# Performance work log

Measured on AMD Instinct MI355X. Metric: run time of the kernel, lower is better.

## Reference

```python
import jax, jax.numpy as jnp
import numpy as np

DIM, N_HEADS, N_KV_HEADS = 2048, 32, 8
HEAD_DIM = DIM // N_HEADS            # 64
KV_REPEAT = N_HEADS // N_KV_HEADS    # 4
ROPE_THETA = 10000.0


def _rope(x, start_pos):
    # x: [B, T, Hx, hd]  (rotate-half / GPT-NeoX style RoPE)
    B, T, Hx, hd = x.shape
    half = hd // 2
    inv_freq = 1.0 / (ROPE_THETA ** (jnp.arange(half, dtype=jnp.float32) / half))
    pos = (start_pos + jnp.arange(T)).astype(jnp.float32)
    ang = pos[:, None] * inv_freq[None, :]            # [T, half]
    cos = jnp.cos(ang)[None, :, None, :]              # [1, T, 1, half]
    sin = jnp.sin(ang)[None, :, None, :]
    x1, x2 = x[..., :half], x[..., half:]
    return jnp.concatenate([x1 * cos - x2 * sin, x1 * sin + x2 * cos], axis=-1).astype(x.dtype)


def setup_inputs() -> dict:
    key = jax.random.key(0)
    ks = jax.random.split(key, 5)
    B, T = 2, 2048
    s = 1.0 / np.sqrt(DIM)
    return {
        "x": jax.random.normal(ks[0], (B, T, DIM), dtype=jnp.float32),
        "Wq": jax.random.normal(ks[1], (DIM, N_HEADS * HEAD_DIM), dtype=jnp.float32) * s,
        "Wk": jax.random.normal(ks[2], (DIM, N_KV_HEADS * HEAD_DIM), dtype=jnp.float32) * s,
        "Wv": jax.random.normal(ks[3], (DIM, N_KV_HEADS * HEAD_DIM), dtype=jnp.float32) * s,
        "Wo": jax.random.normal(ks[4], (DIM, DIM), dtype=jnp.float32) * s,
        "start_pos": 0,
    }


def reference(x, Wq, Wk, Wv, Wo, start_pos):
    B, T, _ = x.shape
    G, R, hd = N_KV_HEADS, KV_REPEAT, HEAD_DIM
    # projections -> [B, T, H, hd]
    Q = (x @ Wq).reshape(B, T, N_HEADS, hd)
    K = (x @ Wk).reshape(B, T, G, hd)
    V = (x @ Wv).reshape(B, T, G, hd)
    Q = _rope(Q, start_pos)
    K = _rope(K, start_pos)
    # GQA: group query heads as (G kv-groups, R repeats) matching repeat_interleave order
    Qg = Q.reshape(B, T, G, R, hd)
    scale = 1.0 / jnp.sqrt(jnp.asarray(hd, dtype=Q.dtype))
    scores = jnp.einsum('bqgrd,bkgd->bgrqk', Qg, K) * scale   # [B,G,R,T,T]
    # causal mask (is_causal=True since T > 1)
    causal = jnp.tril(jnp.ones((T, T), dtype=bool))
    scores = jnp.where(causal[None, None, None, :, :], scores, jnp.finfo(scores.dtype).min)
    attn = jax.nn.softmax(scores, axis=-1)
    out = jnp.einsum('bgrqk,bkgd->bqgrd', attn, V).reshape(B, T, DIM)
    y = out @ Wo
    # original also returns (K, V) with heads-first layout [B, G, T, hd]
    return (y, K.transpose(0, 2, 1, 3), V.transpose(0, 2, 1, 3))
```

## Files before the change

### kernel.cpp

```cpp
#include <hip/hip_runtime.h>
#include <hip/hip_bf16.h>
#include <stdint.h>


typedef __attribute__((ext_vector_type(4))) float f32x4;
typedef __attribute__((ext_vector_type(16))) float f32x16;
typedef __attribute__((ext_vector_type(8))) short sfrag;
typedef __attribute__((ext_vector_type(8))) __bf16 bfrag;
typedef __attribute__((ext_vector_type(4))) unsigned int u32x4;
typedef unsigned short u16;

__device__ __forceinline__ f32x4 mfma16(sfrag a, sfrag b, f32x4 c) {
  return __builtin_amdgcn_mfma_f32_16x16x32_bf16(
      __builtin_bit_cast(bfrag, a), __builtin_bit_cast(bfrag, b), c, 0, 0, 0);
}
__device__ __forceinline__ f32x16 mfma32(sfrag a, sfrag b, f32x16 c) {
  return __builtin_amdgcn_mfma_f32_32x32x16_bf16(
      __builtin_bit_cast(bfrag, a), __builtin_bit_cast(bfrag, b), c, 0, 0, 0);
}
__device__ __forceinline__ u16 f2b(float f) {
  return __builtin_bit_cast(u16, (__bf16)f);
}
__device__ __forceinline__ unsigned pack2(float a, float b) {
  return (unsigned)f2b(a) | ((unsigned)f2b(b) << 16);
}
__device__ __forceinline__ void swap32(unsigned& a, unsigned& b) {
  asm("v_permlane32_swap_b32 %0, %1" : "+v"(a), "+v"(b));
}

#define GAS __attribute__((address_space(1)))
#define LAS __attribute__((address_space(3)))
__device__ __forceinline__ void gll16(const void* g, void* l) {
  __builtin_amdgcn_global_load_lds((GAS unsigned int*)g, (LAS unsigned int*)l, 16, 0, 0);
}

__global__ __launch_bounds__(256) void k_convx(const float* __restrict__ X,
                                               u16* __restrict__ Y, int n) {
  int i = (blockIdx.x * 256 + threadIdx.x) * 4;
  if (i >= n) return;
  float4 v = *(const float4*)(X + i);
  *(ushort4*)(Y + i) = make_ushort4(f2b(v.x), f2b(v.y), f2b(v.z), f2b(v.w));
}

__global__ __launch_bounds__(256) void k_csn(const int* __restrict__ sp,
                                             float2* __restrict__ csn) {
  const int i = blockIdx.x * 256 + threadIdx.x;
  const int t = i >> 5, j = i & 31;
  const float freq = powf(10000.0f, -(float)j * (1.0f / 32.0f));
  const float ang = (float)(sp[0] + t) * freq;
  csn[i] = make_float2(cosf(ang), sinf(ang));
}

__global__ __launch_bounds__(256) void k_convT3(const float* __restrict__ Wq,
                                                const float* __restrict__ Wk,
                                                const float* __restrict__ Wv,
                                                u16* __restrict__ Wt) {
  __shared__ float tile[64][65];
  const int n0g = blockIdx.x * 64;
  const float* W; int N, n0;
  if (n0g < 2048)      { W = Wq; N = 2048; n0 = n0g; }
  else if (n0g < 2560) { W = Wk; N = 512;  n0 = n0g - 2048; }
  else                 { W = Wv; N = 512;  n0 = n0g - 2560; }
  const int k0 = blockIdx.y * 64;
  #pragma unroll
  for (int p = 0; p < 16; ++p) {
    int idx = p * 256 + threadIdx.x;
    int kk = idx >> 6, nn = idx & 63;
    tile[kk][nn] = W[(size_t)(k0 + kk) * N + n0 + nn];
  }
  __syncthreads();
  #pragma unroll
  for (int p = 0; p < 16; ++p) {
    int idx = p * 256 + threadIdx.x;
    int nn = idx >> 6, kk = idx & 63;
    Wt[(size_t)(n0g + nn) * 2048 + k0 + kk] = f2b(tile[kk][nn]);
  }
}

__global__ __launch_bounds__(256) void k_convT(const float* __restrict__ W,
                                               u16* __restrict__ Wt, int N) {
  __shared__ float tile[64][65];
  int n0 = blockIdx.x * 64, k0 = blockIdx.y * 64;
  #pragma unroll
  for (int p = 0; p < 16; ++p) {
    int idx = p * 256 + threadIdx.x;
    int kk = idx >> 6, nn = idx & 63;
    tile[kk][nn] = W[(size_t)(k0 + kk) * N + n0 + nn];
  }
  __syncthreads();
  #pragma unroll
  for (int p = 0; p < 16; ++p) {
    int idx = p * 256 + threadIdx.x;
    int nn = idx >> 6, kk = idx & 63;
    Wt[(size_t)(n0 + nn) * 2048 + k0 + kk] = f2b(tile[kk][nn]);
  }
}

template<int MODE>
__global__ __launch_bounds__(256, 3) void k_gemm128(const u16* __restrict__ A,
                                                    const u16* __restrict__ Bt,
                                                    float* __restrict__ C,
                                                    int N, int K, int GY,
                                                    const float2* __restrict__ csn,
                                                    u16* __restrict__ Qb,
                                                    u16* __restrict__ Kb,
                                                    float* __restrict__ Kout,
                                                    float* __restrict__ Vout) {
  __shared__ u16 lds[16384];
  char* const L = (char*)&lds[0];
  const int tid = threadIdx.x;
  const int q8 = gridDim.x >> 3;
  const int id2 = (blockIdx.x & 7) * q8 + (blockIdx.x >> 3);
  const int by = id2 % GY, bx = id2 / GY;
  const int wid = tid >> 6, lane = tid & 63;
  const int wm = wid >> 1, wn = wid & 1;
  const int l16 = lane & 15, l4 = lane >> 4;
  const size_t K2 = (size_t)K * 2;
  const char* Ab = (const char*)(A + (size_t)(by * 128) * K);
  const char* Bb = (const char*)(Bt + (size_t)(bx * 128) * K);
  const int NT = K >> 6;

  auto stage = [&](const char* gb, int reg, int t) {
    #pragma unroll
    for (int ld = 0; ld < 4; ++ld) {
      const int p = ld * 4096 + tid * 16;
      const int r = p >> 7;
      const int cb = (p & 127) ^ ((r & 7) << 4);
      gll16(gb + (size_t)r * K2 + (size_t)t * 128 + cb, L + reg + p);
    }
  };

  const int swz = (l16 & 7) << 4;
  const int c0 = (l4 * 16) ^ swz;
  const int c1 = (64 + l4 * 16) ^ swz;
  const int aOff = (wm * 64 + l16) * 128;
  const int bOff = 16384 + (wn * 64 + l16) * 128;

  f32x4 acc[4][4];
  #pragma unroll
  for (int m = 0; m < 4; ++m)
    #pragma unroll
    for (int n = 0; n < 4; ++n) acc[m][n] = f32x4{0.f, 0.f, 0.f, 0.f};

  for (int t = 0; t < NT; ++t) {
    stage(Ab, 0, t);
    stage(Bb, 16384, t);
    __syncthreads();
    sfrag a0[4], a1[4], b0[4], b1[4];
    #pragma unroll
    for (int m = 0; m < 4; ++m) {
      a0[m] = *(const sfrag*)(L + aOff + m * 2048 + c0);
      a1[m] = *(const sfrag*)(L + aOff + m * 2048 + c1);
    }
    #pragma unroll
    for (int n = 0; n < 4; ++n) {
      b0[n] = *(const sfrag*)(L + bOff + n * 2048 + c0);
      b1[n] = *(const sfrag*)(L + bOff + n * 2048 + c1);
    }
    #pragma unroll
    for (int m = 0; m < 4; ++m)
      #pragma unroll
      for (int n = 0; n < 4; ++n) {
        acc[m][n] = mfma16(a0[m], b0[n], acc[m][n]);
        acc[m][n] = mfma16(a1[m], b1[n], acc[m][n]);
      }
    __syncthreads();
  }

  if constexpr (MODE == 0) {
    float* Cb = C + (size_t)(by * 128 + wm * 64) * N + bx * 128 + wn * 64;
    #pragma unroll
    for (int m = 0; m < 4; ++m)
      #pragma unroll
      for (int n = 0; n < 4; ++n)
        #pragma unroll
        for (int r = 0; r < 4; ++r)
          Cb[(size_t)(m * 16 + l4 * 4 + r) * N + n * 16 + l16] = acc[m][n][r];
  } else {
    const int head = bx * 2 + wn;
    const int row0 = by * 128 + wm * 64;
    if (head < 40) {
      const float QS = 0.125f * 1.44269504f;
      #pragma unroll
      for (int m = 0; m < 4; ++m)
        #pragma unroll
        for (int r = 0; r < 4; ++r) {
          const int tg = row0 + m * 16 + l4 * 4 + r;
          const int b = tg >> 11, t = tg & 2047;
          #pragma unroll
          for (int n = 0; n < 2; ++n) {
            const int j = n * 16 + l16;
            const float2 cz = csn[t * 32 + j];
            const float x1 = acc[m][n][r], x2 = acc[m][n + 2][r];
            const float o1 = x1 * cz.x - x2 * cz.y;
            const float o2 = x1 * cz.y + x2 * cz.x;
            if (head < 32) {
              const size_t o = (((size_t)b * 32 + head) * 2048 + t) * 64 + j;
              Qb[o] = f2b(o1 * QS);
              Qb[o + 32] = f2b(o2 * QS);
            } else {
              const int g = head - 32;
              const size_t o = (((size_t)b * 8 + g) * 2048 + t) * 64 + j;
              Kb[o] = f2b(o1);  Kb[o + 32] = f2b(o2);
              Kout[o] = o1;     Kout[o + 32] = o2;
            }
          }
        }
    } else {
      const int g = head - 40;
      #pragma unroll
      for (int m = 0; m < 4; ++m)
        #pragma unroll
        for (int r = 0; r < 4; ++r) {
          const int tg = row0 + m * 16 + l4 * 4 + r;
          const int b = tg >> 11, t = tg & 2047;
          const size_t o = (((size_t)b * 8 + g) * 2048 + t) * 64;
          #pragma unroll
          for (int n = 0; n < 4; ++n)
            Vout[o + n * 16 + l16] = acc[m][n][r];
        }
    }
  }
}

__global__ __launch_bounds__(256) void k_vtrans(const float* __restrict__ Vout,
                                                u16* __restrict__ Vt) {
  __shared__ float tile[64][65];
  int t0 = blockIdx.x * 64;
  int bg = blockIdx.y;
  const float* src = Vout + (size_t)bg * (2048 * 64);
  #pragma unroll
  for (int p = 0; p < 16; ++p) {
    int idx = p * 256 + threadIdx.x;
    int tt = idx >> 6, d = idx & 63;
    tile[tt][d] = src[(size_t)(t0 + tt) * 64 + d];
  }
  __syncthreads();
  #pragma unroll
  for (int p = 0; p < 16; ++p) {
    int idx = p * 256 + threadIdx.x;
    int d = idx >> 6, tt = idx & 63;
    Vt[((size_t)bg * 64 + d) * 2048 + t0 + tt] = f2b(tile[tt][d]);
  }
}

__device__ __forceinline__ void pv4(const float* p, sfrag v0a, sfrag v0b,
                                    sfrag v1a, sfrag v1b,
                                    f32x16& O0, f32x16& O1, float& l) {
  unsigned w[8];
  #pragma unroll
  for (int j = 0; j < 8; ++j) w[j] = pack2(p[2 * j], p[2 * j + 1]);
  swap32(w[0], w[2]);
  swap32(w[1], w[3]);
  swap32(w[4], w[6]);
  swap32(w[5], w[7]);
  const sfrag pf0 = __builtin_bit_cast(sfrag, u32x4{w[0], w[1], w[2], w[3]});
  const sfrag pf1 = __builtin_bit_cast(sfrag, u32x4{w[4], w[5], w[6], w[7]});
  O0 = mfma32(v0a, pf0, O0);
  O0 = mfma32(v0b, pf1, O0);
  O1 = mfma32(v1a, pf0, O1);
  O1 = mfma32(v1b, pf1, O1);
  float s[8];
  #pragma unroll
  for (int j = 0; j < 8; ++j) s[j] = p[j] + p[j + 8];
  #pragma unroll
  for (int j = 0; j < 4; ++j) s[j] = s[j] + s[j + 4];
  l += (s[0] + s[1]) + (s[2] + s[3]);
}

__device__ __forceinline__ void tile64_l(const u16* __restrict__ buf,
                                         const sfrag* qf, int hi, int l31, int swz,
                                         f32x16& O0, f32x16& O1, float& l) {
  const char* Kl = (const char*)buf;
  const char* Vl = Kl + 8192;
  const int rb = l31 * 128;
  f32x16 Sa = {}, Sb = {};
  #pragma unroll
  for (int ks = 0; ks < 4; ++ks) {
    const int col = (hi * 16 + ks * 32) ^ swz;
    const sfrag ka = *(const sfrag*)(Kl + rb + col);
    const sfrag kb = *(const sfrag*)(Kl + rb + col + 4096);
    Sa = mfma32(ka, qf[ks], Sa);
    Sb = mfma32(kb, qf[ks], Sb);
  }
  float pa[16], pb[16];
  #pragma unroll
  for (int r = 0; r < 16; ++r) {
    pa[r] = __builtin_amdgcn_exp2f(Sa[r]);
    pb[r] = __builtin_amdgcn_exp2f(Sb[r]);
  }
  sfrag v0[4], v1[4];
  #pragma unroll
  for (int s = 0; s < 4; ++s) {
    const int col = (s * 32 + hi * 16) ^ swz;
    v0[s] = *(const sfrag*)(Vl + rb + col);
    v1[s] = *(const sfrag*)(Vl + rb + col + 4096);
  }
  pv4(pa, v0[0], v0[1], v1[0], v1[1], O0, O1, l);
  pv4(pb, v0[2], v0[3], v1[2], v1[3], O0, O1, l);
}

template<bool MASKED>
__device__ __forceinline__ void tile32_l(const u16* __restrict__ buf, int c,
                                         const sfrag* qf, int hi, int l31, int swz,
                                         f32x16& O0, f32x16& O1, float& l) {
  const char* Kl = (const char*)buf;
  const char* Vl = Kl + 8192;
  const int rb = l31 * 128;
  f32x16 S = {};
  #pragma unroll
  for (int ks = 0; ks < 4; ++ks) {
    const int col = (hi * 16 + ks * 32) ^ swz;
    const sfrag k = *(const sfrag*)(Kl + c * 4096 + rb + col);
    S = mfma32(k, qf[ks], S);
  }
  float p[16];
  #pragma unroll
  for (int r = 0; r < 16; ++r) {
    float s = S[r];
    if (MASKED) {
      int kvo = (r & 3) + 8 * (r >> 2) + 4 * hi;
      if (kvo > l31) s = -__builtin_inff();
    }
    p[r] = __builtin_amdgcn_exp2f(s);
  }
  const int colA = (c * 64 + hi * 16) ^ swz;
  const int colB = (c * 64 + 32 + hi * 16) ^ swz;
  const sfrag v0a = *(const sfrag*)(Vl + rb + colA);
  const sfrag v0b = *(const sfrag*)(Vl + rb + colB);
  const sfrag v1a = *(const sfrag*)(Vl + rb + colA + 4096);
  const sfrag v1b = *(const sfrag*)(Vl + rb + colB + 4096);
  pv4(p, v0a, v0b, v1a, v1b, O0, O1, l);
}

__global__ __launch_bounds__(256, 4) void k_attn5(const u16* __restrict__ Qb,
                                                  const u16* __restrict__ Kb,
                                                  const u16* __restrict__ Vt,
                                                  u16* __restrict__ attOut) {
  __shared__ u16 lds[2][8192];
  const int bid = blockIdx.x;
  const int qb = 63 - (bid >> 4);
  const int bg = bid & 15;
  const int b = bg >> 3, g = bg & 7;
  const int wave = threadIdx.x >> 6, lane = threadIdx.x & 63;
  const int h = g * 4 + wave;
  const int hi = lane >> 5, l31 = lane & 31;
  const int qrow0 = qb * 32;
  const int swz = (l31 & 7) << 4;

  const u16* Qp = Qb + (((size_t)b * 32 + h) * 2048 + qrow0 + l31) * 64 + hi * 8;
  sfrag qf[4];
  #pragma unroll
  for (int ks = 0; ks < 4; ++ks) qf[ks] = *(const sfrag*)(Qp + ks * 16);

  const char* Kg = (const char*)(Kb + ((size_t)b * 8 + g) * (2048 * 64));
  const char* Vg = (const char*)(Vt + ((size_t)b * 8 + g) * (64 * 2048));

  auto stage = [&](int bufi, int t) {
    const char* Ktile = Kg + (size_t)t * 8192;
    const char* Vtile = Vg + t * 128;
    #pragma unroll
    for (int rd = 0; rd < 2; ++rd) {
      const int p = rd * 4096 + threadIdx.x * 16;
      const int d = p >> 7;
      const int cb = (p & 127) ^ ((d & 7) << 4);
      const int lbase = rd * 4096 + wave * 1024;
      gll16(Ktile + d * 128 + cb, (char*)&lds[bufi][0] + lbase);
      gll16(Vtile + (size_t)d * 4096 + cb, (char*)&lds[bufi][0] + 8192 + lbase);
    }
  };

  f32x16 O0 = {}, O1 = {};
  float lsum = 0.f;
  const int nfull = qrow0 >> 6;
  int cur = 0;
  stage(0, 0);
  for (int t = 0; t < nfull; ++t) {
    __syncthreads();
    stage(cur ^ 1, t + 1);
    tile64_l(lds[cur], qf, hi, l31, swz, O0, O1, lsum);
    cur ^= 1;
  }
  __syncthreads();
  if (qb & 1) {
    tile32_l<false>(lds[cur], 0, qf, hi, l31, swz, O0, O1, lsum);
    tile32_l<true>(lds[cur], 1, qf, hi, l31, swz, O0, O1, lsum);
  } else {
    tile32_l<true>(lds[cur], 0, qf, hi, l31, swz, O0, O1, lsum);
  }

  const float ltot = lsum + __shfl_xor(lsum, 32);
  const float inv = 1.0f / ltot;
  const size_t orow = ((size_t)b * 2048 + qrow0 + l31) * 2048 + h * 64;
  #pragma unroll
  for (int dt = 0; dt < 2; ++dt) {
    const f32x16& O = dt ? O1 : O0;
    #pragma unroll
    for (int k = 0; k < 4; ++k) {
      ushort4 o;
      o.x = f2b(O[4 * k + 0] * inv);
      o.y = f2b(O[4 * k + 1] * inv);
      o.z = f2b(O[4 * k + 2] * inv);
      o.w = f2b(O[4 * k + 3] * inv);
      *(ushort4*)&attOut[orow + dt * 32 + 8 * k + 4 * hi] = o;
    }
  }
}

extern "C" void kernel_launch(void* const* d_in, const int* in_sizes, int n_in,
                              void* d_out, int out_size, void* d_ws, size_t ws_size,
                              hipStream_t stream) {
  const float* x  = (const float*)d_in[0];
  const float* Wq = (const float*)d_in[1];
  const float* Wk = (const float*)d_in[2];
  const float* Wv = (const float*)d_in[3];
  const float* Wo = (const float*)d_in[4];
  const int* sp   = (const int*)d_in[5];
  float* y    = (float*)d_out;
  float* Kout = y + 8388608;
  float* Vout = y + 10485760;

  char* ws = (char*)d_ws;
  u16*    xb     = (u16*)(ws + 0);
  u16*    Wqkvt  = (u16*)(ws + 16777216);
  u16*    Wot    = (u16*)(ws + 29360128);
  float2* csn    = (float2*)(ws + 37748736);
  u16*    Qbuf   = (u16*)(ws + 88080384);
  u16*    Kbuf   = (u16*)(ws + 104857600);
  u16*    Vt     = (u16*)(ws + 109051904);
  u16*    attOut = xb;

  k_convx<<<8192, 256, 0, stream>>>(x, xb, 8388608);
  k_csn<<<256, 256, 0, stream>>>(sp, csn);
  k_convT3<<<dim3(48, 32), 256, 0, stream>>>(Wq, Wk, Wv, Wqkvt);
  k_convT<<<dim3(32, 32), 256, 0, stream>>>(Wo, Wot, 2048);
  k_gemm128<1><<<768, 256, 0, stream>>>(xb, Wqkvt, nullptr, 3072, 2048, 32,
                                        csn, Qbuf, Kbuf, Kout, Vout);
  k_vtrans<<<dim3(32, 16), 256, 0, stream>>>(Vout, Vt);
  k_attn5<<<1024, 256, 0, stream>>>(Qbuf, Kbuf, Vt, attOut);
  k_gemm128<0><<<512, 256, 0, stream>>>(attOut, Wot, y, 2048, 2048, 32,
                                        nullptr, nullptr, nullptr, nullptr, nullptr);
}
```

Measured before the change: 186.5 us.

## Merge prep kernels, vectorize weight transpose, stage Q/K epilogue through LDS

Merges the x conversion and RoPE table kernels into one launch, and the three weight transposes into one vectorized kernel using float4 loads and ushort4 stores. The QKV GEMM epilogue now writes rotated Q/K bf16 values to per-wave LDS and then emits coalesced 16-byte global stores instead of scattered 2-byte stores. This cuts launch count and uncoalesced write traffic. In exchange it adds a block-wide sync in the epilogue and reuses LDS assumed free after the main loop.

Result: no change. 184.9 us (-0.9%).

```diff
diff --git a/kernel.cpp b/kernel.cpp
--- a/kernel.cpp
+++ b/kernel.cpp
@@ -35,64 +35,59 @@
 }
 
 __global__ __launch_bounds__(256) void k_convx(const float* __restrict__ X,
-                                               u16* __restrict__ Y, int n) {
-  int i = (blockIdx.x * 256 + threadIdx.x) * 4;
-  if (i >= n) return;
-  float4 v = *(const float4*)(X + i);
-  *(ushort4*)(Y + i) = make_ushort4(f2b(v.x), f2b(v.y), f2b(v.z), f2b(v.w));
-}
-
-__global__ __launch_bounds__(256) void k_csn(const int* __restrict__ sp,
-                                             float2* __restrict__ csn) {
-  const int i = blockIdx.x * 256 + threadIdx.x;
-  const int t = i >> 5, j = i & 31;
-  const float freq = powf(10000.0f, -(float)j * (1.0f / 32.0f));
-  const float ang = (float)(sp[0] + t) * freq;
-  csn[i] = make_float2(cosf(ang), sinf(ang));
-}
-
-__global__ __launch_bounds__(256) void k_convT3(const float* __restrict__ Wq,
-                                                const float* __restrict__ Wk,
-                                                const float* __restrict__ Wv,
-                                                u16* __restrict__ Wt) {
+                                               u16* __restrict__ Y,
+                                               const int* __restrict__ sp,
+                                               float2* __restrict__ csn) {
+  const int bid = blockIdx.x;
+  if (bid < 8192) {
+    const int i = (bid * 256 + threadIdx.x) * 4;
+    float4 v = *(const float4*)(X + i);
+    *(ushort4*)(Y + i) = make_ushort4(f2b(v.x), f2b(v.y), f2b(v.z), f2b(v.w));
+  } else {
+    const int i = (bid - 8192) * 256 + threadIdx.x;
+    const int t = i >> 5, j = i & 31;
+    const float freq = powf(10000.0f, -(float)j * (1.0f / 32.0f));
+    const float ang = (float)(sp[0] + t) * freq;
+    csn[i] = make_float2(cosf(ang), sinf(ang));
+  }
+}
+
+__global__ __launch_bounds__(256) void k_convTall(const float* __restrict__ Wq,
+                                                  const float* __restrict__ Wk,
+                                                  const float* __restrict__ Wv,
+                                                  const float* __restrict__ Wo,
+                                                  u16* __restrict__ Wqkvt,
+                                                  u16* __restrict__ Wot) {
   __shared__ float tile[64][65];
-  const int n0g = blockIdx.x * 64;
-  const float* W; int N, n0;
-  if (n0g < 2048)      { W = Wq; N = 2048; n0 = n0g; }
-  else if (n0g < 2560) { W = Wk; N = 512;  n0 = n0g - 2048; }
-  else                 { W = Wv; N = 512;  n0 = n0g - 2560; }
+  const int bx = blockIdx.x;
   const int k0 = blockIdx.y * 64;
-  #pragma unroll
-  for (int p = 0; p < 16; ++p) {
-    int idx = p * 256 + threadIdx.x;
-    int kk = idx >> 6, nn = idx & 63;
-    tile[kk][nn] = W[(size_t)(k0 + kk) * N + n0 + nn];
+  const float* W; int N, n0; u16* Dst; int nd;
+  if (bx < 32)      { W = Wq; N = 2048; n0 = bx * 64;        Dst = Wqkvt; nd = n0; }
+  else if (bx < 40) { W = Wk; N = 512;  n0 = (bx - 32) * 64; Dst = Wqkvt; nd = 2048 + n0; }
+  else if (bx < 48) { W = Wv; N = 512;  n0 = (bx - 40) * 64; Dst = Wqkvt; nd = 2560 + n0; }
+  else              { W = Wo; N = 2048; n0 = (bx - 48) * 64; Dst = Wot;   nd = n0; }
+  const int tid = threadIdx.x;
+  #pragma unroll
+  for (int it = 0; it < 4; ++it) {
+    const int idx = it * 256 + tid;
+    const int kk = idx >> 4, nq = idx & 15;
+    float4 v = *(const float4*)(W + (size_t)(k0 + kk) * N + n0 + nq * 4);
+    tile[kk][nq * 4 + 0] = v.x;
+    tile[kk][nq * 4 + 1] = v.y;
+    tile[kk][nq * 4 + 2] = v.z;
+    tile[kk][nq * 4 + 3] = v.w;
   }
   __syncthreads();
   #pragma unroll
-  for (int p = 0; p < 16; ++p) {
-    int idx = p * 256 + threadIdx.x;
-    int nn = idx >> 6, kk = idx & 63;
-    Wt[(size_t)(n0g + nn) * 2048 + k0 + kk] = f2b(tile[kk][nn]);
-  }
-}
-
-__global__ __launch_bounds__(256) void k_convT(const float* __restrict__ W,
-                                               u16* __restrict__ Wt, int N) {
-  __shared__ float tile[64][65];
-  int n0 = blockIdx.x * 64, k0 = blockIdx.y * 64;
-  #pragma unroll
-  for (int p = 0; p < 16; ++p) {
-    int idx = p * 256 + threadIdx.x;
-    int kk = idx >> 6, nn = idx & 63;
-    tile[kk][nn] = W[(size_t)(k0 + kk) * N + n0 + nn];
-  }
-  __syncthreads();
-  #pragma unroll
-  for (int p = 0; p < 16; ++p) {
-    int idx = p * 256 + threadIdx.x;
-    int nn = idx >> 6, kk = idx & 63;
-    Wt[(size_t)(n0 + nn) * 2048 + k0 + kk] = f2b(tile[kk][nn]);
+  for (int it = 0; it < 4; ++it) {
+    const int idx = it * 256 + tid;
+    const int nn = idx >> 4, kq = idx & 15;
+    ushort4 o;
+    o.x = f2b(tile[kq * 4 + 0][nn]);
+    o.y = f2b(tile[kq * 4 + 1][nn]);
+    o.z = f2b(tile[kq * 4 + 2][nn]);
+    o.w = f2b(tile[kq * 4 + 3][nn]);
+    *(ushort4*)(Dst + (size_t)(nd + nn) * 2048 + k0 + kq * 4) = o;
   }
 }
 
@@ -180,12 +175,15 @@
     const int head = bx * 2 + wn;
     const int row0 = by * 128 + wm * 64;
     if (head < 40) {
+      u16* Lw = (u16*)(L + wid * 8192);
       const float QS = 0.125f * 1.44269504f;
+      const bool isQ = head < 32;
       #pragma unroll
       for (int m = 0; m < 4; ++m)
         #pragma unroll
         for (int r = 0; r < 4; ++r) {
-          const int tg = row0 + m * 16 + l4 * 4 + r;
+          const int tl = m * 16 + l4 * 4 + r;
+          const int tg = row0 + tl;
           const int b = tg >> 11, t = tg & 2047;
           #pragma unroll
           for (int n = 0; n < 2; ++n) {
@@ -194,18 +192,31 @@
             const float x1 = acc[m][n][r], x2 = acc[m][n + 2][r];
             const float o1 = x1 * cz.x - x2 * cz.y;
             const float o2 = x1 * cz.y + x2 * cz.x;
-            if (head < 32) {
-              const size_t o = (((size_t)b * 32 + head) * 2048 + t) * 64 + j;
-              Qb[o] = f2b(o1 * QS);
-              Qb[o + 32] = f2b(o2 * QS);
+            if (isQ) {
+              Lw[tl * 64 + j]      = f2b(o1 * QS);
+              Lw[tl * 64 + j + 32] = f2b(o2 * QS);
             } else {
+              Lw[tl * 64 + j]      = f2b(o1);
+              Lw[tl * 64 + j + 32] = f2b(o2);
               const int g = head - 32;
               const size_t o = (((size_t)b * 8 + g) * 2048 + t) * 64 + j;
-              Kb[o] = f2b(o1);  Kb[o + 32] = f2b(o2);
-              Kout[o] = o1;     Kout[o + 32] = o2;
+              Kout[o] = o1;  Kout[o + 32] = o2;
             }
           }
         }
+      __syncthreads();
+      u16* dst = isQ ? Qb : Kb;
+      const int hh = isQ ? head : (head - 32);
+      const int hstride = isQ ? 32 : 8;
+      #pragma unroll
+      for (int it = 0; it < 8; ++it) {
+        const int tl = it * 8 + (lane >> 3);
+        const int col = (lane & 7) * 8;
+        const u32x4 v = *(const u32x4*)&Lw[tl * 64 + col];
+        const int tg = row0 + tl;
+        const int b = tg >> 11, t = tg & 2047;
+        *(u32x4*)(dst + (((size_t)b * hstride + hh) * 2048 + t) * 64 + col) = v;
+      }
     } else {
       const int g = head - 40;
       #pragma unroll
@@ -430,10 +441,8 @@
   u16*    Vt     = (u16*)(ws + 109051904);
   u16*    attOut = xb;
 
-  k_convx<<<8192, 256, 0, stream>>>(x, xb, 8388608);
-  k_csn<<<256, 256, 0, stream>>>(sp, csn);
-  k_convT3<<<dim3(48, 32), 256, 0, stream>>>(Wq, Wk, Wv, Wqkvt);
-  k_convT<<<dim3(32, 32), 256, 0, stream>>>(Wo, Wot, 2048);
+  k_convx<<<8448, 256, 0, stream>>>(x, xb, sp, csn);
+  k_convTall<<<dim3(80, 32), 256, 0, stream>>>(Wq, Wk, Wv, Wo, Wqkvt, Wot);
   k_gemm128<1><<<768, 256, 0, stream>>>(xb, Wqkvt, nullptr, 3072, 2048, 32,
                                         csn, Qbuf, Kbuf, Kout, Vout);
   k_vtrans<<<dim3(32, 16), 256, 0, stream>>>(Vout, Vt);
```
